# Kernel optimization log

Measured on AMD Instinct MI355X. Metric: run time of the kernel, lower is better.

Reference implementation:

```python
import jax, jax.numpy as jnp
import numpy as np

EMBED_DIM = 1024
N1 = 4096
N2 = 4096


def setup_inputs() -> dict:
    key = jax.random.key(0)
    ks = jax.random.split(key, 14)
    s = 1.0 / np.sqrt(EMBED_DIM)
    def lin(k):
        kw, kb = jax.random.split(k)
        W = jax.random.uniform(kw, (EMBED_DIM, EMBED_DIM), jnp.float32, -s, s)
        b = jax.random.uniform(kb, (EMBED_DIM,), jnp.float32, -s, s)
        return W, b
    Wq1, bq1 = lin(ks[0]); Wk1, bk1 = lin(ks[1]); Wv1, bv1 = lin(ks[2])
    Wq2, bq2 = lin(ks[3]); Wk2, bk2 = lin(ks[4]); Wv2, bv2 = lin(ks[5])
    x1 = jax.random.normal(ks[6], (N1, EMBED_DIM), jnp.float32)
    x2 = jax.random.normal(ks[7], (N2, EMBED_DIM), jnp.float32)
    return {
        "input_tensor1": x1, "input_tensor2": x2,
        "Wq1": Wq1, "bq1": bq1, "Wk1": Wk1, "bk1": bk1, "Wv1": Wv1, "bv1": bv1,
        "Wq2": Wq2, "bq2": bq2, "Wk2": Wk2, "bk2": bk2, "Wv2": Wv2, "bv2": bv2,
    }


def reference(input_tensor1, input_tensor2,
              Wq1, bq1, Wk1, bk1, Wv1, bv1,
              Wq2, bq2, Wk2, bk2, Wv2, bv2):
    scale = 1.0 / jnp.sqrt(jnp.asarray(EMBED_DIM, input_tensor1.dtype))
    # torch Linear: y = x @ W.T + b
    q1 = input_tensor1 @ Wq1.T + bq1   # [N1, D]
    k1 = input_tensor1 @ Wk1.T + bk1
    v1 = input_tensor1 @ Wv1.T + bv1
    q2 = input_tensor2 @ Wq2.T + bq2   # [N2, D]
    k2 = input_tensor2 @ Wk2.T + bk2
    v2 = input_tensor2 @ Wv2.T + bv2
    # stream-2 queries attend over stream-1 keys/values
    scores1 = (q2 @ k1.T) * scale                  # [N2, N1]
    probs1 = jax.nn.softmax(scores1, axis=-1)      # dropout p=0 -> identity
    context1 = probs1 @ v1                         # [N2, D]
    # stream-1 queries attend over stream-2 keys/values
    scores2 = (q1 @ k2.T) * scale                  # [N1, N2]
    probs2 = jax.nn.softmax(scores2, axis=-1)
    context2 = probs2 @ v2                         # [N1, D]
    return (context1, context2)
```

## Files before the change

### kernel.cpp

```cpp
#include <hip/hip_runtime.h>
#include <hip/hip_bf16.h>
#include <cstdint>
#include <cstddef>

#define DEVINL __device__ __forceinline__

typedef __attribute__((ext_vector_type(4))) float   f32x4;
typedef __bf16 bf16x8 __attribute__((ext_vector_type(8)));
typedef __attribute__((ext_vector_type(4))) short   short4v;
typedef __attribute__((ext_vector_type(4))) float   float4v;

static constexpr int DIM = 1024;
static constexpr int NTOK = 4096;

DEVINL unsigned short f2bf(float f) {
  unsigned u = __float_as_uint(f);
  u += 0x7FFF + ((u >> 16) & 1);
  return (unsigned short)(u >> 16);
}
DEVINL float bf2f(unsigned short s) {
  return __uint_as_float(((unsigned)s) << 16);
}

DEVINL void gll16(const void* g, void* l) {
  __builtin_amdgcn_global_load_lds(
      (const __attribute__((address_space(1))) void*)g,
      (__attribute__((address_space(3))) void*)l, 16, 0, 0);
}

DEVINL void core256(const unsigned short* __restrict__ A, int lda,
                    const unsigned short* __restrict__ B, int ldb,
                    int K, int brow, int bcol, f32x4 acc[8][4])
{
  __shared__ unsigned short lds[65536];
  const int t = threadIdx.x;
  const int w = t >> 6, l = t & 63;
  const int wr = w >> 2, wc = w & 3;
  const int srow = l >> 3;
  const int scol = ((l & 7) ^ srow) << 3;
  const int l15 = l & 15;
  const int cs0 = (((l >> 4) << 3)       ^ ((l & 7) << 3));
  const int cs1 = ((32 + ((l >> 4) << 3)) ^ ((l & 7) << 3));

  const unsigned short* aL = A + (size_t)(brow * 256 + srow) * lda + scol;
  const unsigned short* bL = B + (size_t)(bcol * 256 + srow) * ldb + scol;

#pragma unroll
  for (int m = 0; m < 8; ++m)
#pragma unroll
    for (int n = 0; n < 4; ++n) {
      f32x4 z = {0.f, 0.f, 0.f, 0.f};
      acc[m][n] = z;
    }

#define STA_(Sbase, h, r, kt)                                                  \
  gll16(aL + (size_t)((r)*128 + (h)*64 + (w << 3)) * lda + (size_t)(kt)*64,    \
        (Sbase) + ((r)*128 + (h)*64 + (w << 3)) * 64)
#define STB_(Sbase, h, r, kt)                                                  \
  { const int g16_ = w + (r)*8;                                                \
    const int r0_ = (g16_ >> 2)*64 + (h)*32 + (g16_ & 3)*8;                    \
    gll16(bL + (size_t)r0_ * ldb + (size_t)(kt)*64, (Sbase) + r0_ * 64); }
#define LDA_(Abase, mh)                                                        \
  _Pragma("unroll")                                                            \
  for (int m4 = 0; m4 < 4; ++m4) {                                             \
    const unsigned short* p_ = (Abase) + (wr*128 + (mh)*64 + m4*16 + l15)*64;  \
    af[m4][0] = *(const bf16x8*)(p_ + cs0);                                    \
    af[m4][1] = *(const bf16x8*)(p_ + cs1);                                    \
  }
#define LDB_(Bbase, nh)                                                        \
  _Pragma("unroll")                                                            \
  for (int n2 = 0; n2 < 2; ++n2) {                                             \
    const unsigned short* p_ = (Bbase) + (wc*64 + (nh)*32 + n2*16 + l15)*64;   \
    bfr[n2][0] = *(const bf16x8*)(p_ + cs0);                                   \
    bfr[n2][1] = *(const bf16x8*)(p_ + cs1);                                   \
  }
#define MF_(mh, nh)                                                            \
  __builtin_amdgcn_s_setprio(1);                                               \
  _Pragma("unroll")                                                            \
  for (int m4 = 0; m4 < 4; ++m4)                                               \
  _Pragma("unroll")                                                            \
  for (int n2 = 0; n2 < 2; ++n2) {                                             \
    f32x4 c_ = acc[(mh)*4 + m4][(nh)*2 + n2];                                  \
    c_ = __builtin_amdgcn_mfma_f32_16x16x32_bf16(af[m4][0], bfr[n2][0], c_, 0,0,0); \
    c_ = __builtin_amdgcn_mfma_f32_16x16x32_bf16(af[m4][1], bfr[n2][1], c_, 0,0,0); \
    acc[(mh)*4 + m4][(nh)*2 + n2] = c_;                                        \
  }                                                                            \
  __builtin_amdgcn_s_setprio(0);
#define VMW4() asm volatile("s_waitcnt vmcnt(4)" ::: "memory")
#define VMW0() asm volatile("s_waitcnt vmcnt(0)" ::: "memory")
#define LGW()  do { asm volatile("s_waitcnt lgkmcnt(0)" ::: "memory");         \
                    __builtin_amdgcn_sched_barrier(0); } while (0)
#define BARR() do { __builtin_amdgcn_s_barrier();                              \
                    asm volatile("" ::: "memory"); } while (0)

  {
    unsigned short* S0  = lds;
    unsigned short* S0b = lds + 16384;
    STA_(S0, 0, 0, 0); STA_(S0, 0, 1, 0); STB_(S0b, 0, 0, 0); STB_(S0b, 0, 1, 0);
    STA_(S0, 1, 0, 0); STA_(S0, 1, 1, 0); STB_(S0b, 1, 0, 0); STB_(S0b, 1, 1, 0);
  }

  bf16x8 af[4][2], bfr[2][2];
  const int NT = K >> 6;
  for (int kt = 0; kt < NT - 1; ++kt) {
    const unsigned short* Ab = lds + (kt & 1) * 32768;
    const unsigned short* Bb = Ab + 16384;
    unsigned short* Sa = lds + ((kt & 1) ^ 1) * 32768;
    unsigned short* Sb = Sa + 16384;

    VMW4(); BARR();
    STA_(Sa, 0, 0, kt + 1); STA_(Sa, 0, 1, kt + 1);
    STB_(Sb, 0, 0, kt + 1); STB_(Sb, 0, 1, kt + 1);
    LDA_(Ab, 0); LDB_(Bb, 0);
    LGW(); MF_(0, 0);

    VMW4(); BARR();
    STA_(Sa, 1, 0, kt + 1); STA_(Sa, 1, 1, kt + 1);
    STB_(Sb, 1, 0, kt + 1); STB_(Sb, 1, 1, kt + 1);
    LDA_(Ab, 1);
    LGW(); MF_(1, 0);

    LDB_(Bb, 1);
    LGW(); MF_(1, 1);

    LDA_(Ab, 0);
    LGW(); MF_(0, 1);
  }

  {
    const int kt = NT - 1;
    const unsigned short* Ab = lds + (kt & 1) * 32768;
    const unsigned short* Bb = Ab + 16384;
    VMW4(); BARR();
    LDA_(Ab, 0); LDB_(Bb, 0);
    LGW(); MF_(0, 0);
    VMW0(); BARR();
    LDA_(Ab, 1);
    LGW(); MF_(1, 0);
    LDB_(Bb, 1);
    LGW(); MF_(1, 1);
    LDA_(Ab, 0);
    LGW(); MF_(0, 1);
  }
#undef STA_
#undef STB_
#undef LDA_
#undef LDB_
#undef MF_
#undef VMW4
#undef VMW0
#undef LGW
#undef BARR
}

__global__ __launch_bounds__(512, 2)
void gemm256_scores(const unsigned short* __restrict__ A,
                    const unsigned short* __restrict__ B,
                    unsigned short* __restrict__ S, float scale)
{
  f32x4 acc[8][4];
  core256(A, DIM, B, DIM, DIM, blockIdx.y, blockIdx.x, acc);

  const int t = threadIdx.x, w = t >> 6, l = t & 63;
  const int wr = w >> 2, wc = w & 3;
  const int r4 = (l >> 4) * 4, c = l & 15;
  const int row0 = blockIdx.y * 256 + wr * 128;
  const int col0 = blockIdx.x * 256 + wc * 64;
#pragma unroll
  for (int mf = 0; mf < 8; ++mf)
#pragma unroll
    for (int nf = 0; nf < 4; ++nf)
#pragma unroll
      for (int i = 0; i < 4; ++i)
        S[(size_t)(row0 + mf*16 + r4 + i) * NTOK + col0 + nf*16 + c] =
            f2bf(acc[mf][nf][i] * scale);
}

__global__ __launch_bounds__(512, 2)
void qkv256(const unsigned short* __restrict__ x1, const unsigned short* __restrict__ x2,
            const unsigned short* __restrict__ W6,
            const float* bq1, const float* bk1, const float* bv1,
            const float* bq2, const float* bk2, const float* bv2,
            unsigned short* q1, unsigned short* k1, unsigned short* v1T,
            unsigned short* q2, unsigned short* k2, unsigned short* v2T)
{
  const int g = blockIdx.z;
  const unsigned short* A = (g < 3) ? x1 : x2;
  const unsigned short* W = W6 + (size_t)g * (DIM * DIM);
  const float* bias = (g == 0) ? bq1 : (g == 1) ? bk1 : (g == 2) ? bv1
                    : (g == 3) ? bq2 : (g == 4) ? bk2 : bv2;
  unsigned short* out = (g == 0) ? q1 : (g == 1) ? k1 : (g == 2) ? v1T
                      : (g == 3) ? q2 : (g == 4) ? k2 : v2T;
  const bool vT = (g == 2 || g == 5);

  f32x4 acc[8][4];
  core256(A, DIM, W, DIM, DIM, blockIdx.y, blockIdx.x, acc);

  const int t = threadIdx.x, w = t >> 6, l = t & 63;
  const int wr = w >> 2, wc = w & 3;
  const int r4 = (l >> 4) * 4, c = l & 15;
  const int row0 = blockIdx.y * 256 + wr * 128;
  const int col0 = blockIdx.x * 256 + wc * 64;

  float bias_v[4];
#pragma unroll
  for (int nf = 0; nf < 4; ++nf) bias_v[nf] = bias[col0 + nf*16 + c];

  if (!vT) {
#pragma unroll
    for (int mf = 0; mf < 8; ++mf)
#pragma unroll
      for (int nf = 0; nf < 4; ++nf)
#pragma unroll
        for (int i = 0; i < 4; ++i)
          out[(size_t)(row0 + mf*16 + r4 + i) * DIM + col0 + nf*16 + c] =
              f2bf(acc[mf][nf][i] + bias_v[nf]);
  } else {
#pragma unroll
    for (int mf = 0; mf < 8; ++mf)
#pragma unroll
      for (int nf = 0; nf < 4; ++nf) {
        short4v pk;
#pragma unroll
        for (int i = 0; i < 4; ++i) pk[i] = (short)f2bf(acc[mf][nf][i] + bias_v[nf]);
        *(short4v*)(out + (size_t)(col0 + nf*16 + c) * NTOK + row0 + mf*16 + r4) = pk;
      }
  }
}

__global__ __launch_bounds__(512, 2)
void pv_fused(const unsigned short* __restrict__ S1,
              const unsigned short* __restrict__ S2,
              const unsigned short* __restrict__ vTcat,
              float* __restrict__ out, float* __restrict__ P)
{
  const int bx = blockIdx.x, by = blockIdx.y, z = blockIdx.z;
  const unsigned short* A = ((bx < 4) ? S1 : S2) + (size_t)z * 2048;
  const unsigned short* B = vTcat + (size_t)z * 2048;

  f32x4 acc[8][4];
  core256(A, NTOK, B, NTOK, 2048, by, bx, acc);

  const int t = threadIdx.x, w = t >> 6, l = t & 63;
  const int wr = w >> 2, wc = w & 3;
  const int r4 = (l >> 4) * 4, c = l & 15;
  const int row0 = by * 256 + wr * 128;
  const int col0 = bx * 256 + wc * 64;

#pragma unroll
  for (int mf = 0; mf < 8; ++mf)
#pragma unroll
    for (int nf = 0; nf < 4; ++nf)
#pragma unroll
      for (int i = 0; i < 4; ++i) {
        const int r = row0 + mf*16 + r4 + i;
        const int cg = col0 + nf*16 + c;
        if (z) {
          P[(size_t)r * 2048 + cg] = acc[mf][nf][i];
        } else {
          float* dst = (cg < 1024) ? (out + (size_t)r * 1024 + cg)
                                   : (out + 4194304 + (size_t)r * 1024 + (cg - 1024));
          *dst = acc[mf][nf][i];
        }
      }
}

__global__ __launch_bounds__(256)
void add_pv(float* __restrict__ out, const float* __restrict__ P)
{
  const int idx = blockIdx.x * 256 + threadIdx.x;
  const int r  = idx >> 9;
  const int c4 = (idx & 511) << 2;
  const float4v p = *(const float4v*)(P + (size_t)r * 2048 + c4);
  float* dst = (c4 < 1024) ? (out + (size_t)r * 1024 + c4)
                           : (out + 4194304 + (size_t)r * 1024 + (c4 - 1024));
  float4v a = *(const float4v*)dst;
#pragma unroll
  for (int j = 0; j < 4; ++j) a[j] += p[j];
  *(float4v*)dst = a;
}

__global__ __launch_bounds__(256)
void softmax_inplace(unsigned short* __restrict__ S)
{
  const int row = blockIdx.x;
  unsigned short* r = S + (size_t)row * NTOK;
  const int t = threadIdx.x, wave = t >> 6, lane = t & 63;
  __shared__ float red[4];

  bf16x8 d0 = *(const bf16x8*)(r + t * 8);
  bf16x8 d1 = *(const bf16x8*)(r + 2048 + t * 8);
  float v[16];
  {
    const unsigned short* p0 = (const unsigned short*)&d0;
    const unsigned short* p1 = (const unsigned short*)&d1;
#pragma unroll
    for (int j = 0; j < 8; ++j) { v[j] = bf2f(p0[j]); v[8 + j] = bf2f(p1[j]); }
  }
  float mx = v[0];
#pragma unroll
  for (int j = 1; j < 16; ++j) mx = fmaxf(mx, v[j]);
#pragma unroll
  for (int o = 32; o > 0; o >>= 1) mx = fmaxf(mx, __shfl_xor(mx, o));
  if (lane == 0) red[wave] = mx;
  __syncthreads();
  mx = fmaxf(fmaxf(red[0], red[1]), fmaxf(red[2], red[3]));

  float s = 0.f;
#pragma unroll
  for (int j = 0; j < 16; ++j) { v[j] = __expf(v[j] - mx); s += v[j]; }
#pragma unroll
  for (int o = 32; o > 0; o >>= 1) s += __shfl_xor(s, o);
  __syncthreads();
  if (lane == 0) red[wave] = s;
  __syncthreads();
  s = red[0] + red[1] + red[2] + red[3];
  const float inv = 1.0f / s;

  unsigned short o0[8], o1[8];
#pragma unroll
  for (int j = 0; j < 8; ++j) { o0[j] = f2bf(v[j] * inv); o1[j] = f2bf(v[8 + j] * inv); }
  *(bf16x8*)(r + t * 8)        = *(const bf16x8*)o0;
  *(bf16x8*)(r + 2048 + t * 8) = *(const bf16x8*)o1;
}

__global__ __launch_bounds__(256)
void cvt2(const float* __restrict__ a, const float* __restrict__ b,
          unsigned short* __restrict__ oa, unsigned short* __restrict__ ob)
{
  const float* in = blockIdx.y ? b : a;
  unsigned short* out = blockIdx.y ? ob : oa;
  const size_t i = ((size_t)blockIdx.x * 256 + threadIdx.x) * 4;
  float4v x = *(const float4v*)(in + i);
  short4v o;
#pragma unroll
  for (int j = 0; j < 4; ++j) o[j] = (short)f2bf(x[j]);
  *(short4v*)(out + i) = o;
}

__global__ __launch_bounds__(256)
void cvt_w(const float* w0, const float* w1, const float* w2,
           const float* w3, const float* w4, const float* w5,
           unsigned short* __restrict__ W6)
{
  const float* srcs[6] = {w0, w1, w2, w3, w4, w5};
  const float* in = srcs[blockIdx.y];
  unsigned short* out = W6 + (size_t)blockIdx.y * (DIM * DIM);
  const size_t i = ((size_t)blockIdx.x * 256 + threadIdx.x) * 4;
  float4v x = *(const float4v*)(in + i);
  short4v o;
#pragma unroll
  for (int j = 0; j < 4; ++j) o[j] = (short)f2bf(x[j]);
  *(short4v*)(out + i) = o;
}

extern "C" void kernel_launch(void* const* d_in, const int* in_sizes, int n_in,
                              void* d_out, int out_size, void* d_ws, size_t ws_size,
                              hipStream_t stream)
{
  const float* x1  = (const float*)d_in[0];
  const float* x2  = (const float*)d_in[1];
  const float* Wq1 = (const float*)d_in[2];  const float* bq1 = (const float*)d_in[3];
  const float* Wk1 = (const float*)d_in[4];  const float* bk1 = (const float*)d_in[5];
  const float* Wv1 = (const float*)d_in[6];  const float* bv1 = (const float*)d_in[7];
  const float* Wq2 = (const float*)d_in[8];  const float* bq2 = (const float*)d_in[9];
  const float* Wk2 = (const float*)d_in[10]; const float* bk2 = (const float*)d_in[11];
  const float* Wv2 = (const float*)d_in[12]; const float* bv2 = (const float*)d_in[13];
  float* out = (float*)d_out;

  unsigned short* ws  = (unsigned short*)d_ws;
  const size_t NTD = (size_t)NTOK * DIM;
  const size_t SM  = (size_t)NTOK * NTOK;
  unsigned short* x1b = ws;
  unsigned short* x2b = x1b + NTD;
  unsigned short* W6  = x2b + NTD;
  unsigned short* S1  = ws;
  unsigned short* S2  = ws + SM;
  unsigned short* q1  = ws + 2 * SM;
  unsigned short* k1  = q1 + NTD;
  unsigned short* q2  = k1 + NTD;
  unsigned short* k2  = q2 + NTD;
  unsigned short* vT  = k2 + NTD;
  unsigned short* v1T = vT;
  unsigned short* v2T = vT + NTD;
  float* P = (float*)q1;

  const dim3 blk(256);
  cvt2 <<<dim3(NTD / 1024, 2), blk, 0, stream>>>(x1, x2, x1b, x2b);
  cvt_w<<<dim3((DIM * DIM) / 1024, 6), blk, 0, stream>>>(Wq1, Wk1, Wv1, Wq2, Wk2, Wv2, W6);

  qkv256<<<dim3(DIM / 256, NTOK / 256, 6), dim3(512), 0, stream>>>(
      x1b, x2b, W6, bq1, bk1, bv1, bq2, bk2, bv2, q1, k1, v1T, q2, k2, v2T);

  const float scale = 0.03125f;

  gemm256_scores<<<dim3(NTOK / 256, NTOK / 256), dim3(512), 0, stream>>>(q2, k1, S1, scale);
  softmax_inplace<<<dim3(NTOK), blk, 0, stream>>>(S1);
  gemm256_scores<<<dim3(NTOK / 256, NTOK / 256), dim3(512), 0, stream>>>(q1, k2, S2, scale);
  softmax_inplace<<<dim3(NTOK), blk, 0, stream>>>(S2);

  pv_fused<<<dim3(8, NTOK / 256, 2), dim3(512), 0, stream>>>(S1, S2, vT, out, P);
  add_pv<<<dim3(8192), blk, 0, stream>>>(out, P);
}
```

Before: 261.0 us.

## Restructure GEMM mainloop into eight-slot LDS ring with finer-grained prefetch

Replaces the two-stage double-buffered K loop with an eight-slot LDS ring of 8192-element half-tiles. Each A/B half-tile is loaded into its own slot up to two k-tiles ahead, and a barrier sits around each quarter of the MFMA work so slots are freed and refilled at half-tile granularity. B fragments are kept in two register sets so the four MFMA quadrants can reuse them. The goal is deeper overlap of global-to-LDS traffic with MFMA. The cost is many more barriers per tile and intricate slot and vmcnt bookkeeping that could be wrong.

Result: no change. 265.3 us (+1.7%).

```diff
diff --git a/kernel.cpp b/kernel.cpp
--- a/kernel.cpp
+++ b/kernel.cpp
@@ -39,7 +39,7 @@
   const int srow = l >> 3;
   const int scol = ((l & 7) ^ srow) << 3;
   const int l15 = l & 15;
-  const int cs0 = (((l >> 4) << 3)       ^ ((l & 7) << 3));
+  const int cs0 = (((l >> 4) << 3)        ^ ((l & 7) << 3));
   const int cs1 = ((32 + ((l >> 4) << 3)) ^ ((l & 7) << 3));
 
   const unsigned short* aL = A + (size_t)(brow * 256 + srow) * lda + scol;
@@ -53,102 +53,93 @@
       acc[m][n] = z;
     }
 
-#define STA_(Sbase, h, r, kt)                                                  \
+#define STA(slot, h, r, kt)                                                    \
   gll16(aL + (size_t)((r)*128 + (h)*64 + (w << 3)) * lda + (size_t)(kt)*64,    \
-        (Sbase) + ((r)*128 + (h)*64 + (w << 3)) * 64)
-#define STB_(Sbase, h, r, kt)                                                  \
+        lds + (slot)*8192 + ((r)*64 + (w << 3)) * 64)
+#define STB(slot, h, r, kt)                                                    \
   { const int g16_ = w + (r)*8;                                                \
-    const int r0_ = (g16_ >> 2)*64 + (h)*32 + (g16_ & 3)*8;                    \
-    gll16(bL + (size_t)r0_ * ldb + (size_t)(kt)*64, (Sbase) + r0_ * 64); }
-#define LDA_(Abase, mh)                                                        \
+    gll16(bL + (size_t)((g16_>>2)*64 + (h)*32 + (g16_&3)*8) * ldb              \
+              + (size_t)(kt)*64,                                               \
+          lds + (slot)*8192 + ((g16_>>2)*32 + (g16_&3)*8) * 64); }
+#define LDAm(dst, slot)                                                        \
   _Pragma("unroll")                                                            \
   for (int m4 = 0; m4 < 4; ++m4) {                                             \
-    const unsigned short* p_ = (Abase) + (wr*128 + (mh)*64 + m4*16 + l15)*64;  \
-    af[m4][0] = *(const bf16x8*)(p_ + cs0);                                    \
-    af[m4][1] = *(const bf16x8*)(p_ + cs1);                                    \
-  }
-#define LDB_(Bbase, nh)                                                        \
+    const unsigned short* p_ = lds + (slot)*8192 + (wr*64 + m4*16 + l15)*64;   \
+    dst[m4][0] = *(const bf16x8*)(p_ + cs0);                                   \
+    dst[m4][1] = *(const bf16x8*)(p_ + cs1);                                   \
+  }
+#define LDBm(dst, slot)                                                        \
   _Pragma("unroll")                                                            \
   for (int n2 = 0; n2 < 2; ++n2) {                                             \
-    const unsigned short* p_ = (Bbase) + (wc*64 + (nh)*32 + n2*16 + l15)*64;   \
-    bfr[n2][0] = *(const bf16x8*)(p_ + cs0);                                   \
-    bfr[n2][1] = *(const bf16x8*)(p_ + cs1);                                   \
-  }
-#define MF_(mh, nh)                                                            \
+    const unsigned short* p_ = lds + (slot)*8192 + (wc*32 + n2*16 + l15)*64;   \
+    dst[n2][0] = *(const bf16x8*)(p_ + cs0);                                   \
+    dst[n2][1] = *(const bf16x8*)(p_ + cs1);                                   \
+  }
+#define MF(mh, nh, br)                                                         \
   __builtin_amdgcn_s_setprio(1);                                               \
   _Pragma("unroll")                                                            \
   for (int m4 = 0; m4 < 4; ++m4)                                               \
   _Pragma("unroll")                                                            \
   for (int n2 = 0; n2 < 2; ++n2) {                                             \
     f32x4 c_ = acc[(mh)*4 + m4][(nh)*2 + n2];                                  \
-    c_ = __builtin_amdgcn_mfma_f32_16x16x32_bf16(af[m4][0], bfr[n2][0], c_, 0,0,0); \
-    c_ = __builtin_amdgcn_mfma_f32_16x16x32_bf16(af[m4][1], bfr[n2][1], c_, 0,0,0); \
+    c_ = __builtin_amdgcn_mfma_f32_16x16x32_bf16(af[m4][0], br[n2][0], c_, 0,0,0); \
+    c_ = __builtin_amdgcn_mfma_f32_16x16x32_bf16(af[m4][1], br[n2][1], c_, 0,0,0); \
     acc[(mh)*4 + m4][(nh)*2 + n2] = c_;                                        \
   }                                                                            \
   __builtin_amdgcn_s_setprio(0);
-#define VMW4() asm volatile("s_waitcnt vmcnt(4)" ::: "memory")
-#define VMW0() asm volatile("s_waitcnt vmcnt(0)" ::: "memory")
 #define LGW()  do { asm volatile("s_waitcnt lgkmcnt(0)" ::: "memory");         \
                     __builtin_amdgcn_sched_barrier(0); } while (0)
-#define BARR() do { __builtin_amdgcn_s_barrier();                              \
+#define BARR() do { asm volatile("" ::: "memory");                             \
+                    __builtin_amdgcn_s_barrier();                              \
                     asm volatile("" ::: "memory"); } while (0)
 
-  {
-    unsigned short* S0  = lds;
-    unsigned short* S0b = lds + 16384;
-    STA_(S0, 0, 0, 0); STA_(S0, 0, 1, 0); STB_(S0b, 0, 0, 0); STB_(S0b, 0, 1, 0);
-    STA_(S0, 1, 0, 0); STA_(S0, 1, 1, 0); STB_(S0b, 1, 0, 0); STB_(S0b, 1, 1, 0);
-  }
-
-  bf16x8 af[4][2], bfr[2][2];
   const int NT = K >> 6;
-  for (int kt = 0; kt < NT - 1; ++kt) {
-    const unsigned short* Ab = lds + (kt & 1) * 32768;
-    const unsigned short* Bb = Ab + 16384;
-    unsigned short* Sa = lds + ((kt & 1) ^ 1) * 32768;
-    unsigned short* Sb = Sa + 16384;
-
-    VMW4(); BARR();
-    STA_(Sa, 0, 0, kt + 1); STA_(Sa, 0, 1, kt + 1);
-    STB_(Sb, 0, 0, kt + 1); STB_(Sb, 0, 1, kt + 1);
-    LDA_(Ab, 0); LDB_(Bb, 0);
-    LGW(); MF_(0, 0);
-
-    VMW4(); BARR();
-    STA_(Sa, 1, 0, kt + 1); STA_(Sa, 1, 1, kt + 1);
-    STB_(Sb, 1, 0, kt + 1); STB_(Sb, 1, 1, kt + 1);
-    LDA_(Ab, 1);
-    LGW(); MF_(1, 0);
-
-    LDB_(Bb, 1);
-    LGW(); MF_(1, 1);
-
-    LDA_(Ab, 0);
-    LGW(); MF_(0, 1);
-  }
-
-  {
-    const int kt = NT - 1;
-    const unsigned short* Ab = lds + (kt & 1) * 32768;
-    const unsigned short* Bb = Ab + 16384;
-    VMW4(); BARR();
-    LDA_(Ab, 0); LDB_(Bb, 0);
-    LGW(); MF_(0, 0);
-    VMW0(); BARR();
-    LDA_(Ab, 1);
-    LGW(); MF_(1, 0);
-    LDB_(Bb, 1);
-    LGW(); MF_(1, 1);
-    LDA_(Ab, 0);
-    LGW(); MF_(0, 1);
-  }
-#undef STA_
-#undef STB_
-#undef LDA_
-#undef LDB_
-#undef MF_
-#undef VMW4
-#undef VMW0
+
+  STA(1, 0, 0, 0); STA(1, 0, 1, 0);
+  STB(2, 1, 0, 0); STB(2, 1, 1, 0);
+  STA(3, 1, 0, 0); STA(3, 1, 1, 0);
+  STB(4, 0, 0, 0); STB(4, 0, 1, 0);
+  STA(5, 0, 0, 1); STA(5, 0, 1, 1);
+  STB(6, 1, 0, 1); STB(6, 1, 1, 1);
+  STA(7, 1, 0, 1); STA(7, 1, 1, 1);
+  asm volatile("s_waitcnt vmcnt(6)" ::: "memory");
+  BARR();
+
+  bf16x8 af[4][2], b0r[2][2], b1r[2][2];
+
+#define TILE(kt, sA0, sB1, sA1, sB0, nB0, nA0, nB1, nA1)                       \
+  {                                                                            \
+                                                              \
+    LDAm(af, sA0);                                                             \
+    LDBm(b0r, sB0);                                                            \
+    if ((kt) + 1 < NT) { STB(nB0, 0, 0, (kt)+1); STB(nB0, 0, 1, (kt)+1); }     \
+    asm volatile("s_waitcnt lgkmcnt(8)" ::: "memory");                         \
+    BARR(); LGW(); MF(0, 0, b0r); BARR();                                      \
+                                                              \
+    LDBm(b1r, sB1);                                                            \
+    if ((kt) + 2 < NT) { STA(nA0, 0, 0, (kt)+2); STA(nA0, 0, 1, (kt)+2); }     \
+    BARR(); LGW(); MF(0, 1, b1r); BARR();                                      \
+                                                              \
+    LDAm(af, sA1);                                                             \
+    if ((kt) + 2 < NT) { STB(nB1, 1, 0, (kt)+2); STB(nB1, 1, 1, (kt)+2); }     \
+    BARR(); LGW(); MF(1, 1, b1r); BARR();                                      \
+                                 \
+    if ((kt) + 2 < NT) { STA(nA1, 1, 0, (kt)+2); STA(nA1, 1, 1, (kt)+2); }     \
+    if ((kt) + 2 >= NT) { asm volatile("s_waitcnt vmcnt(0)" ::: "memory"); }   \
+    else                { asm volatile("s_waitcnt vmcnt(6)" ::: "memory"); }   \
+    BARR(); MF(1, 0, b0r); BARR();                                             \
+  }
+
+  for (int kt = 0; kt < NT; kt += 2) {
+    TILE(kt,     1, 2, 3, 4,  0, 1, 2, 3);
+    TILE(kt + 1, 5, 6, 7, 0,  4, 5, 6, 7);
+  }
+#undef TILE
+#undef STA
+#undef STB
+#undef LDAm
+#undef LDBm
+#undef MF
 #undef LGW
 #undef BARR
 }
```
